# Kernel optimization log

Hardware: AMD Instinct MI355X
Metric: run time of the kernel (lower is better)

Reference implementation:

```python
import jax, jax.numpy as jnp
import numpy as np
from jax import lax

GAMMA = 2        # unused in forward (kept for fidelity to source)
PW = 10.0
THRESHOLD = 1.0
ERODE = 3
BACKZERO = 0

B, C, D, H, W = 2, 1, 128, 256, 256


def setup_inputs() -> dict:
    key = jax.random.key(0)
    k1, k2 = jax.random.split(key)
    inp = jax.random.normal(k1, (B, C, D, H, W), dtype=jnp.float32)
    tgt = jax.random.uniform(k2, (B, C, D, H, W), dtype=jnp.float32)
    return {"input": inp, "target": tgt}


def _box_sum_3d(x, r):
    # All-ones (2r+1)^3 conv3d with padding=r == sliding-window sum (shape-preserving).
    k = 2 * r + 1
    return lax.reduce_window(
        x, 0.0, lax.add,
        window_dimensions=(1, 1, k, k, k),
        window_strides=(1, 1, 1, 1, 1),
        padding=[(0, 0), (0, 0), (r, r), (r, r), (r, r)],
    )


def reference(input, target):
    # weight = clamp(target, 0, threshold); zero out voxels exactly at threshold
    w = jnp.clip(target, 0.0, THRESHOLD)
    w = w - THRESHOLD * (w == THRESHOLD).astype(jnp.float32)
    # box-filter "erosion" then binarize
    w = _box_sum_3d(w, ERODE)
    w = (w > 0).astype(jnp.float32)
    w = 1.0 + w * PW
    if BACKZERO != 0:
        mask = (input < 0).astype(jnp.float32) * (target == 0).astype(jnp.float32)
        w = w * (1.0 - mask)
    loss = jnp.abs(target - input) * w
    return jnp.mean(loss)
```

## Files before the change

### kernel.cpp

```cpp
#include <hip/hip_runtime.h>
#include <stdint.h>

#define BB 2
#define DD 128
#define HH 256
#define WW 256
static constexpr int64_t N = (int64_t)BB * DD * HH * WW;
static constexpr int WPR    = WW / 64;
static constexpr int NWORDS = BB * DD * HH * WPR;
static constexpr int RBLOCKS = 4096;

__global__ __launch_bounds__(256) void mask_xdil(const float* __restrict__ tgt,
                                                 uint64_t* __restrict__ mask) {
    const int wave = threadIdx.x >> 6;
    const int lane = threadIdx.x & 63;
    const int row  = blockIdx.x * 4 + wave;

    float4 t = ((const float4*)(tgt + (int64_t)row * WW))[lane];

    const uint64_t W0 = __ballot(t.x > 0.0f && t.x < 1.0f);
    const uint64_t W1 = __ballot(t.y > 0.0f && t.y < 1.0f);
    const uint64_t W2 = __ballot(t.z > 0.0f && t.z < 1.0f);
    const uint64_t W3 = __ballot(t.w > 0.0f && t.w < 1.0f);

    const uint64_t U  = W0 | W1 | W2 | W3;
    const uint64_t D0 = U | ((W1 | W2 | W3) << 1);
    const uint64_t D1 = U | ((W2 | W3) << 1) | (W0 >> 1);
    const uint64_t D2 = U | (W3 << 1) | ((W0 | W1) >> 1);
    const uint64_t D3 = U | ((W0 | W1 | W2) >> 1);

    uint64_t d = D0;
    if (lane == 1) d = D1;
    if (lane == 2) d = D2;
    if (lane == 3) d = D3;
    if (lane < 4)
        mask[(int64_t)row * WPR + lane] = d;
}

__device__ __forceinline__ uint64_t spread4(uint64_t x) {
    x &= 0xFFFFull;
    x = (x | (x << 24)) & 0x000000FF000000FFull;
    x = (x | (x << 12)) & 0x000F000F000F000Full;
    x = (x | (x << 6))  & 0x0303030303030303ull;
    x = (x | (x << 3))  & 0x1111111111111111ull;
    return x;
}

__global__ __launch_bounds__(256) void yz_dil(const uint64_t* __restrict__ in,
                                              uint64_t* __restrict__ out) {
    __shared__ uint64_t raw[4][22][23];
    __shared__ uint64_t yd[4][22][17];
    const int ty = threadIdx.x & 15;
    const int tz = threadIdx.x >> 4;
    const int y0 = blockIdx.x * 16;
    const int z0 = blockIdx.y * 16;
    const int b  = blockIdx.z;

    for (int idx = threadIdx.x; idx < 22 * 22; idx += 256) {
        const int zz = idx / 22, yy = idx % 22;
        const int gz = z0 - 3 + zz, gy = y0 - 3 + yy;
        const bool ok = (gz >= 0 && gz < DD && gy >= 0 && gy < HH);
        const uint64_t* p = in + (((int64_t)(b * DD + gz)) * HH + gy) * WPR;
        #pragma unroll
        for (int j = 0; j < 4; j++)
            raw[j][zz][yy] = ok ? p[j] : 0ull;
    }
    __syncthreads();

    for (int idx = threadIdx.x; idx < 22 * 16; idx += 256) {
        const int zz = idx >> 4, yy = idx & 15;
        #pragma unroll
        for (int j = 0; j < 4; j++) {
            uint64_t v = 0;
            #pragma unroll
            for (int d = 0; d < 7; d++) v |= raw[j][zz][yy + d];
            yd[j][zz][yy] = v;
        }
    }
    __syncthreads();

    uint64_t D[4];
    #pragma unroll
    for (int j = 0; j < 4; j++) {
        uint64_t v = 0;
        #pragma unroll
        for (int d = 0; d < 7; d++) v |= yd[j][tz + d][ty];
        D[j] = v;
    }

    uint64_t* o = out + (((int64_t)(b * DD + z0 + tz)) * HH + y0 + ty) * WPR;
    #pragma unroll
    for (int wx = 0; wx < 4; wx++) {
        uint64_t r = 0;
        #pragma unroll
        for (int j = 0; j < 4; j++)
            r |= spread4(D[j] >> (16 * wx)) << j;
        o[wx] = r;
    }
}

__global__ __launch_bounds__(256) void reduce_loss(const float* __restrict__ inp,
                                                   const float* __restrict__ tgt,
                                                   const uint64_t* __restrict__ mask,
                                                   double* __restrict__ partials) {
    const int64_t nvec = N / 4;
    const int64_t stride = (int64_t)RBLOCKS * 256;
    float local = 0.0f;
    for (int64_t i = (int64_t)blockIdx.x * 256 + threadIdx.x; i < nvec; i += stride) {
        float4 a = ((const float4*)inp)[i];
        float4 t = ((const float4*)tgt)[i];
        uint64_t w = mask[i >> 4];
        unsigned nib = (unsigned)(w >> ((i & 15) * 4)) & 0xFu;
        float s;
        s  = fabsf(t.x - a.x) * ((nib & 1u) ? 11.0f : 1.0f);
        s += fabsf(t.y - a.y) * ((nib & 2u) ? 11.0f : 1.0f);
        s += fabsf(t.z - a.z) * ((nib & 4u) ? 11.0f : 1.0f);
        s += fabsf(t.w - a.w) * ((nib & 8u) ? 11.0f : 1.0f);
        local += s;
    }
    #pragma unroll
    for (int off = 32; off > 0; off >>= 1)
        local += __shfl_down(local, off, 64);
    __shared__ float wsum[4];
    const int lane = threadIdx.x & 63;
    const int wv   = threadIdx.x >> 6;
    if (lane == 0) wsum[wv] = local;
    __syncthreads();
    if (threadIdx.x == 0)
        partials[blockIdx.x] = (double)(wsum[0] + wsum[1] + wsum[2] + wsum[3]);
}

__global__ __launch_bounds__(1024) void finalize(const double* __restrict__ partials,
                                                 float* __restrict__ out) {
    double local = 0.0;
    for (int i = threadIdx.x; i < RBLOCKS; i += 1024) local += partials[i];
    #pragma unroll
    for (int off = 32; off > 0; off >>= 1)
        local += __shfl_down(local, off, 64);
    __shared__ double ws[16];
    const int lane = threadIdx.x & 63;
    const int wv   = threadIdx.x >> 6;
    if (lane == 0) ws[wv] = local;
    __syncthreads();
    if (threadIdx.x == 0) {
        double s = 0.0;
        #pragma unroll
        for (int k = 0; k < 16; k++) s += ws[k];
        out[0] = (float)(s / (double)N);
    }
}

extern "C" void kernel_launch(void* const* d_in, const int* in_sizes, int n_in,
                              void* d_out, int out_size, void* d_ws, size_t ws_size,
                              hipStream_t stream) {
    const float* inp = (const float*)d_in[0];
    const float* tgt = (const float*)d_in[1];
    float* out = (float*)d_out;

    double*   partials = (double*)d_ws;
    uint64_t* mask0 = (uint64_t*)((char*)d_ws + 64 * 1024);
    uint64_t* mask1 = mask0 + NWORDS;

    mask_xdil<<<16384, 256, 0, stream>>>(tgt, mask0);
    yz_dil<<<dim3(HH / 16, DD / 16, BB), 256, 0, stream>>>(mask0, mask1);
    reduce_loss<<<RBLOCKS, 256, 0, stream>>>(inp, tgt, mask1, partials);
    finalize<<<1, 1024, 0, stream>>>(partials, out);
}
```

Baseline: 151.5 us.

## Fuse mask, dilation, loss reduction and finalize into one cooperative kernel

Replaces the four-kernel pipeline with a single cooperative kernel of 1024 blocks that separates the x-dilation, yz-dilation, loss reduction and final sum phases with grid-wide syncs. The goal is to remove kernel-launch gaps and tail effects between stages. The yz-dilation phase now runs on only 256 blocks and processes one mask word per pass with smaller shared arrays, so most of the grid idles during that phase. The old multi-kernel path is kept as a fallback if the cooperative launch fails.

```diff
diff --git a/kernel.cpp b/kernel.cpp
--- a/kernel.cpp
+++ b/kernel.cpp
@@ -1,5 +1,8 @@
 #include <hip/hip_runtime.h>
+#include <hip/hip_cooperative_groups.h>
 #include <stdint.h>
+
+namespace cg = cooperative_groups;
 
 #define BB 2
 #define DD 128
@@ -10,32 +13,11 @@
 static constexpr int NWORDS = BB * DD * HH * WPR;
 static constexpr int RBLOCKS = 4096;
 
-__global__ __launch_bounds__(256) void mask_xdil(const float* __restrict__ tgt,
-                                                 uint64_t* __restrict__ mask) {
-    const int wave = threadIdx.x >> 6;
-    const int lane = threadIdx.x & 63;
-    const int row  = blockIdx.x * 4 + wave;
-
-    float4 t = ((const float4*)(tgt + (int64_t)row * WW))[lane];
-
-    const uint64_t W0 = __ballot(t.x > 0.0f && t.x < 1.0f);
-    const uint64_t W1 = __ballot(t.y > 0.0f && t.y < 1.0f);
-    const uint64_t W2 = __ballot(t.z > 0.0f && t.z < 1.0f);
-    const uint64_t W3 = __ballot(t.w > 0.0f && t.w < 1.0f);
-
-    const uint64_t U  = W0 | W1 | W2 | W3;
-    const uint64_t D0 = U | ((W1 | W2 | W3) << 1);
-    const uint64_t D1 = U | ((W2 | W3) << 1) | (W0 >> 1);
-    const uint64_t D2 = U | (W3 << 1) | ((W0 | W1) >> 1);
-    const uint64_t D3 = U | ((W0 | W1 | W2) >> 1);
-
-    uint64_t d = D0;
-    if (lane == 1) d = D1;
-    if (lane == 2) d = D2;
-    if (lane == 3) d = D3;
-    if (lane < 4)
-        mask[(int64_t)row * WPR + lane] = d;
-}
+static constexpr int GRID = 1024;
+static constexpr int TPB  = 256;
+static constexpr int NWAVES = GRID * (TPB / 64);
+static constexpr int ROWS = BB * DD * HH;
+static constexpr int ROWS_PER_WAVE = ROWS / NWAVES;
 
 __device__ __forceinline__ uint64_t spread4(uint64_t x) {
     x &= 0xFFFFull;
@@ -44,6 +26,156 @@
     x = (x | (x << 6))  & 0x0303030303030303ull;
     x = (x | (x << 3))  & 0x1111111111111111ull;
     return x;
+}
+
+__global__ __launch_bounds__(TPB, 4) void fused_all(
+    const float* __restrict__ inp, const float* __restrict__ tgt,
+    uint64_t* __restrict__ mask0, uint64_t* __restrict__ mask1,
+    double* __restrict__ partials, float* __restrict__ out)
+{
+    cg::grid_group grid = cg::this_grid();
+    __shared__ uint64_t raw[22][23];
+    __shared__ uint64_t yd[22][17];
+    __shared__ float  wsum[4];
+    __shared__ double dsum[4];
+
+    const int tid  = threadIdx.x;
+    const int wave = tid >> 6;
+    const int lane = tid & 63;
+    const int gw   = blockIdx.x * 4 + wave;
+
+    #pragma unroll
+    for (int k = 0; k < ROWS_PER_WAVE; k += 4) {
+        float4 t[4];
+        #pragma unroll
+        for (int u = 0; u < 4; u++) {
+            const int row = gw + (k + u) * NWAVES;
+            t[u] = ((const float4*)(tgt + (int64_t)row * WW))[lane];
+        }
+        #pragma unroll
+        for (int u = 0; u < 4; u++) {
+            const int row = gw + (k + u) * NWAVES;
+            const uint64_t W0 = __ballot(t[u].x > 0.0f && t[u].x < 1.0f);
+            const uint64_t W1 = __ballot(t[u].y > 0.0f && t[u].y < 1.0f);
+            const uint64_t W2 = __ballot(t[u].z > 0.0f && t[u].z < 1.0f);
+            const uint64_t W3 = __ballot(t[u].w > 0.0f && t[u].w < 1.0f);
+            const uint64_t U  = W0 | W1 | W2 | W3;
+            const uint64_t D0 = U | ((W1 | W2 | W3) << 1);
+            const uint64_t D1 = U | ((W2 | W3) << 1) | (W0 >> 1);
+            const uint64_t D2 = U | (W3 << 1) | ((W0 | W1) >> 1);
+            const uint64_t D3 = U | ((W0 | W1 | W2) >> 1);
+            uint64_t d = D0;
+            if (lane == 1) d = D1;
+            if (lane == 2) d = D2;
+            if (lane == 3) d = D3;
+            if (lane < 4) mask0[(int64_t)row * WPR + lane] = d;
+        }
+    }
+    grid.sync();
+
+    if (blockIdx.x < 256) {
+        const int ty = tid & 15, tz = tid >> 4;
+        const int y0 = (blockIdx.x & 15) * 16;
+        const int z0 = ((blockIdx.x >> 4) & 7) * 16;
+        const int b  = blockIdx.x >> 7;
+
+        uint64_t D[4];
+        #pragma unroll
+        for (int j = 0; j < 4; j++) {
+            for (int idx = tid; idx < 22 * 22; idx += TPB) {
+                const int zz = idx / 22, yy = idx % 22;
+                const int gz = z0 - 3 + zz, gy = y0 - 3 + yy;
+                const bool ok = (gz >= 0 && gz < DD && gy >= 0 && gy < HH);
+                uint64_t v = 0;
+                if (ok) v = mask0[(((int64_t)(b * DD + gz)) * HH + gy) * WPR + j];
+                raw[zz][yy] = v;
+            }
+            __syncthreads();
+            for (int idx = tid; idx < 22 * 16; idx += TPB) {
+                const int zz = idx >> 4, yy = idx & 15;
+                uint64_t v = 0;
+                #pragma unroll
+                for (int d = 0; d < 7; d++) v |= raw[zz][yy + d];
+                yd[zz][yy] = v;
+            }
+            __syncthreads();
+            uint64_t v = 0;
+            #pragma unroll
+            for (int d = 0; d < 7; d++) v |= yd[tz + d][ty];
+            D[j] = v;
+            __syncthreads();
+        }
+        uint64_t* o = mask1 + (((int64_t)(b * DD + z0 + tz)) * HH + y0 + ty) * WPR;
+        #pragma unroll
+        for (int wx = 0; wx < 4; wx++) {
+            uint64_t r = 0;
+            #pragma unroll
+            for (int j = 0; j < 4; j++) r |= spread4(D[j] >> (16 * wx)) << j;
+            o[wx] = r;
+        }
+    }
+    grid.sync();
+
+    static constexpr int64_t GSTRIDE = (int64_t)GRID * TPB;
+    static constexpr int KITER = (int)((N / 4) / GSTRIDE);
+    const int64_t gtid = (int64_t)blockIdx.x * TPB + tid;
+    float local = 0.0f;
+    #pragma unroll 2
+    for (int k = 0; k < KITER; k++) {
+        const int64_t i = gtid + (int64_t)k * GSTRIDE;
+        float4 a = ((const float4*)inp)[i];
+        float4 t = ((const float4*)tgt)[i];
+        uint64_t w = mask1[i >> 4];
+        unsigned nib = (unsigned)(w >> ((i & 15) * 4)) & 0xFu;
+        float s;
+        s  = fabsf(t.x - a.x) * ((nib & 1u) ? 11.0f : 1.0f);
+        s += fabsf(t.y - a.y) * ((nib & 2u) ? 11.0f : 1.0f);
+        s += fabsf(t.z - a.z) * ((nib & 4u) ? 11.0f : 1.0f);
+        s += fabsf(t.w - a.w) * ((nib & 8u) ? 11.0f : 1.0f);
+        local += s;
+    }
+    #pragma unroll
+    for (int off = 32; off > 0; off >>= 1)
+        local += __shfl_down(local, off, 64);
+    if (lane == 0) wsum[wave] = local;
+    __syncthreads();
+    if (tid == 0)
+        partials[blockIdx.x] = (double)((wsum[0] + wsum[1]) + (wsum[2] + wsum[3]));
+    grid.sync();
+
+    if (blockIdx.x == 0) {
+        double loc = 0.0;
+        for (int i = tid; i < GRID; i += TPB) loc += partials[i];
+        #pragma unroll
+        for (int off = 32; off > 0; off >>= 1)
+            loc += __shfl_down(loc, off, 64);
+        if (lane == 0) dsum[wave] = loc;
+        __syncthreads();
+        if (tid == 0)
+            out[0] = (float)(((dsum[0] + dsum[1]) + (dsum[2] + dsum[3])) / (double)N);
+    }
+}
+
+__global__ __launch_bounds__(256) void mask_xdil(const float* __restrict__ tgt,
+                                                 uint64_t* __restrict__ mask) {
+    const int wave = threadIdx.x >> 6;
+    const int lane = threadIdx.x & 63;
+    const int row  = blockIdx.x * 4 + wave;
+    float4 t = ((const float4*)(tgt + (int64_t)row * WW))[lane];
+    const uint64_t W0 = __ballot(t.x > 0.0f && t.x < 1.0f);
+    const uint64_t W1 = __ballot(t.y > 0.0f && t.y < 1.0f);
+    const uint64_t W2 = __ballot(t.z > 0.0f && t.z < 1.0f);
+    const uint64_t W3 = __ballot(t.w > 0.0f && t.w < 1.0f);
+    const uint64_t U  = W0 | W1 | W2 | W3;
+    const uint64_t D0 = U | ((W1 | W2 | W3) << 1);
+    const uint64_t D1 = U | ((W2 | W3) << 1) | (W0 >> 1);
+    const uint64_t D2 = U | (W3 << 1) | ((W0 | W1) >> 1);
+    const uint64_t D3 = U | ((W0 | W1 | W2) >> 1);
+    uint64_t d = D0;
+    if (lane == 1) d = D1;
+    if (lane == 2) d = D2;
+    if (lane == 3) d = D3;
+    if (lane < 4) mask[(int64_t)row * WPR + lane] = d;
 }
 
 __global__ __launch_bounds__(256) void yz_dil(const uint64_t* __restrict__ in,
@@ -55,18 +187,15 @@
     const int y0 = blockIdx.x * 16;
     const int z0 = blockIdx.y * 16;
     const int b  = blockIdx.z;
-
     for (int idx = threadIdx.x; idx < 22 * 22; idx += 256) {
         const int zz = idx / 22, yy = idx % 22;
         const int gz = z0 - 3 + zz, gy = y0 - 3 + yy;
         const bool ok = (gz >= 0 && gz < DD && gy >= 0 && gy < HH);
         const uint64_t* p = in + (((int64_t)(b * DD + gz)) * HH + gy) * WPR;
         #pragma unroll
-        for (int j = 0; j < 4; j++)
-            raw[j][zz][yy] = ok ? p[j] : 0ull;
-    }
-    __syncthreads();
-
+        for (int j = 0; j < 4; j++) raw[j][zz][yy] = ok ? p[j] : 0ull;
+    }
+    __syncthreads();
     for (int idx = threadIdx.x; idx < 22 * 16; idx += 256) {
         const int zz = idx >> 4, yy = idx & 15;
         #pragma unroll
@@ -78,7 +207,6 @@
         }
     }
     __syncthreads();
-
     uint64_t D[4];
     #pragma unroll
     for (int j = 0; j < 4; j++) {
@@ -87,14 +215,12 @@
         for (int d = 0; d < 7; d++) v |= yd[j][tz + d][ty];
         D[j] = v;
     }
-
     uint64_t* o = out + (((int64_t)(b * DD + z0 + tz)) * HH + y0 + ty) * WPR;
     #pragma unroll
     for (int wx = 0; wx < 4; wx++) {
         uint64_t r = 0;
         #pragma unroll
-        for (int j = 0; j < 4; j++)
-            r |= spread4(D[j] >> (16 * wx)) << j;
+        for (int j = 0; j < 4; j++) r |= spread4(D[j] >> (16 * wx)) << j;
         o[wx] = r;
     }
 }
@@ -161,8 +287,13 @@
     uint64_t* mask0 = (uint64_t*)((char*)d_ws + 64 * 1024);
     uint64_t* mask1 = mask0 + NWORDS;
 
-    mask_xdil<<<16384, 256, 0, stream>>>(tgt, mask0);
-    yz_dil<<<dim3(HH / 16, DD / 16, BB), 256, 0, stream>>>(mask0, mask1);
-    reduce_loss<<<RBLOCKS, 256, 0, stream>>>(inp, tgt, mask1, partials);
-    finalize<<<1, 1024, 0, stream>>>(partials, out);
-}
+    void* args[] = {&inp, &tgt, &mask0, &mask1, &partials, &out};
+    hipError_t e = hipLaunchCooperativeKernel((const void*)fused_all, dim3(GRID),
+                                              dim3(TPB), args, 0, stream);
+    if (e != hipSuccess) {
+        mask_xdil<<<16384, 256, 0, stream>>>(tgt, mask0);
+        yz_dil<<<dim3(HH / 16, DD / 16, BB), 256, 0, stream>>>(mask0, mask1);
+        reduce_loss<<<RBLOCKS, 256, 0, stream>>>(inp, tgt, mask1, partials);
+        finalize<<<1, 1024, 0, stream>>>(partials, out);
+    }
+}
```

After: 491.0 us. 3.24x slower.
